# Optimization experiments

Measured on AMD Instinct MI355X. Metric: run time of the kernel, lower is better.

Reference implementation:

```python
import jax, jax.numpy as jnp
import numpy as np

T, B, H, L = 200, 32, 1024, 2
DROPOUT = 0.32
KEEP = 1.0 - DROPOUT
FORGET_GATE_BIAS = 1.0


def setup_inputs() -> dict:
    key = jax.random.key(0)
    ks = jax.random.split(key, 8)
    scale = 1.0 / np.sqrt(H)  # torch LSTM default init: U(-1/sqrt(H), 1/sqrt(H))
    x = jax.random.normal(ks[0], (T, B, H), jnp.float32)
    W_ih = jax.random.uniform(ks[1], (L, 4 * H, H), jnp.float32, -scale, scale)
    W_hh = jax.random.uniform(ks[2], (L, 4 * H, H), jnp.float32, -scale, scale)
    b_ih = jax.random.uniform(ks[3], (L, 4 * H), jnp.float32, -scale, scale)
    b_hh = jax.random.uniform(ks[4], (L, 4 * H), jnp.float32, -scale, scale)
    # forget-gate bias init as in LstmDrop.__init__ (gate order i,f,g,o)
    b_ih = b_ih.at[:, H:2 * H].set(FORGET_GATE_BIAS)
    b_hh = b_hh.at[:, H:2 * H].set(0.0)
    h0 = jnp.zeros((L, B, H), jnp.float32)
    c0 = jnp.zeros((L, B, H), jnp.float32)
    # inverted dropout masks: inter-layer (torch LSTM dropout, applied to all but last layer)
    # and the trailing inplace Dropout on the output sequence
    mask_inter = (jax.random.bernoulli(ks[5], KEEP, (L - 1, T, B, H)) / KEEP).astype(jnp.float32)
    mask_out = (jax.random.bernoulli(ks[6], KEEP, (T, B, H)) / KEEP).astype(jnp.float32)
    return {"x": x, "h0": h0, "c0": c0, "W_ih": W_ih, "W_hh": W_hh,
            "b_ih": b_ih, "b_hh": b_hh, "mask_inter": mask_inter, "mask_out": mask_out}


def _lstm_layer(xs, h, c, Wih, Whh, b):
    # xs: [T,B,in]; Wih/Whh: [4H,in]/[4H,H]; b: [4H] (b_ih + b_hh fused)
    def step(carry, x_t):
        h, c = carry
        gates = x_t @ Wih.T + h @ Whh.T + b  # [B,4H]
        i, f, g, o = jnp.split(gates, 4, axis=-1)
        c = jax.nn.sigmoid(f) * c + jax.nn.sigmoid(i) * jnp.tanh(g)
        h = jax.nn.sigmoid(o) * jnp.tanh(c)
        return (h, c), h
    (hT, cT), ys = jax.lax.scan(step, (h, c), xs)
    return ys, hT, cT


def reference(x, h0, c0, W_ih, W_hh, b_ih, b_hh, mask_inter, mask_out):
    y = x
    h_last, c_last = [], []
    for l in range(L):
        y, hT, cT = _lstm_layer(y, h0[l], c0[l], W_ih[l], W_hh[l], b_ih[l] + b_hh[l])
        h_last.append(hT)
        c_last.append(cT)
        if l < L - 1:  # torch LSTM applies dropout between layers only
            y = y * mask_inter[l]
    y = y * mask_out  # the inplace Dropout on the output sequence
    return y, jnp.stack(h_last), jnp.stack(c_last)
```

## Files before the change

kernel.cpp:

```cpp
#include <hip/hip_runtime.h>

#define T_STEPS 200
#define BATCH   32
#define HID     1024
#define NWG     256
#define NTHR    512

typedef _Float16 half8 __attribute__((ext_vector_type(8)));
typedef float    f32x4 __attribute__((ext_vector_type(4)));

__device__ __forceinline__ void st_coh16(_Float16* p, half8 v) {
    union { half8 h; unsigned long long u[2]; } r; r.h = v;
    unsigned long long* q = (unsigned long long*)p;
    __hip_atomic_store(q,     r.u[0], __ATOMIC_RELAXED, __HIP_MEMORY_SCOPE_AGENT);
    __hip_atomic_store(q + 1, r.u[1], __ATOMIC_RELAXED, __HIP_MEMORY_SCOPE_AGENT);
}

__device__ __forceinline__ half8 cvt8(const float* p) {
    f32x4 lo = *(const f32x4*)p;
    f32x4 hi = *(const f32x4*)(p + 4);
    half8 a;
    a[0] = (_Float16)lo[0]; a[1] = (_Float16)lo[1];
    a[2] = (_Float16)lo[2]; a[3] = (_Float16)lo[3];
    a[4] = (_Float16)hi[0]; a[5] = (_Float16)hi[1];
    a[6] = (_Float16)hi[2]; a[7] = (_Float16)hi[3];
    return a;
}

__global__ void init_k(const float* __restrict__ h0,
                       _Float16* __restrict__ h0b, _Float16* __restrict__ h1b,
                       unsigned* __restrict__ flag0, unsigned* __restrict__ flag1) {
    int i = blockIdx.x * blockDim.x + threadIdx.x;
    if (i < BATCH * HID) {
        h0b[i] = (_Float16)h0[i];
        h1b[i] = (_Float16)h0[BATCH * HID + i];
    }
    if (blockIdx.x == 0) {
        if (threadIdx.x < 128)      flag0[threadIdx.x * 32] = 0;
        else if (threadIdx.x < 256) flag1[(threadIdx.x - 128) * 32] = 0;
    }
}

__global__ __launch_bounds__(NTHR, 2) void lstm_main(
    const float* __restrict__ x, const float* __restrict__ c0,
    const float* __restrict__ Wih, const float* __restrict__ Whh,
    const float* __restrict__ bih, const float* __restrict__ bhh,
    const float* __restrict__ mi, const float* __restrict__ mo,
    float* __restrict__ out,
    _Float16* __restrict__ y0m, _Float16* __restrict__ h0b,
    _Float16* __restrict__ h1b, unsigned* __restrict__ flag0,
    unsigned* __restrict__ flag1)
{
    __shared__ _Float16 W_s[32 * 2048];
    __shared__ float scr[8][2][16][17];
    __shared__ float c_s[BATCH][8];
    __shared__ alignas(16) _Float16 st_h[BATCH][8];
    __shared__ alignas(16) _Float16 st_y[BATCH][8];
    __shared__ float st_o[BATCH][8];

    const int bid   = blockIdx.x;
    const int layer = bid >> 7;
    const int wgl   = bid & 127;
    const int tid   = threadIdx.x;

    const float* WihL = Wih + (size_t)layer * 4 * HID * HID;
    const float* WhhL = Whh + (size_t)layer * 4 * HID * HID;
    for (int idx = tid; idx < 32 * 2048; idx += NTHR) {
        int r = idx >> 11, k = idx & 2047;
        int grow = (r >> 3) * HID + wgl * 8 + (r & 7);
        float v = (k < HID) ? WihL[(size_t)grow * HID + k]
                            : WhhL[(size_t)grow * HID + (k - HID)];
        W_s[idx ^ ((r & 7) << 3)] = (_Float16)v;
    }

    float bias0 = 0.f, bias1 = 0.f, bias2 = 0.f, bias3 = 0.f;
    int b_ = 0, col_ = 0, gcol = 0;
    if (tid < 256) {
        b_ = tid >> 3; col_ = tid & 7; gcol = wgl * 8 + col_;
        bias0 = bih[layer * 4096 + gcol]           + bhh[layer * 4096 + gcol];
        bias1 = bih[layer * 4096 + HID + gcol]     + bhh[layer * 4096 + HID + gcol];
        bias2 = bih[layer * 4096 + 2 * HID + gcol] + bhh[layer * 4096 + 2 * HID + gcol];
        bias3 = bih[layer * 4096 + 3 * HID + gcol] + bhh[layer * 4096 + 3 * HID + gcol];
        c_s[b_][col_] = c0[((size_t)layer * BATCH + b_) * HID + gcol];
    }
    const int ot = tid - 256;
    const int b2 = (ot >= 0) ? (ot >> 3) : 0, c2 = (ot >= 0) ? (ot & 7) : 0;
    const int gcol2 = wgl * 8 + c2;
    __syncthreads();

    const int lane = tid & 63, wid = tid >> 6;
    int kq;
    if (layer == 0) kq = (wid < 4) ? (2 + (wid >> 1)) : ((wid - 4) >> 1);
    else            kq = wid >> 1;
    const int mm   = wid & 1;
    const int srow = kq * 2 + mm;
    const int row = lane & 15, bb = mm * 16 + row, ko = (lane >> 4) * 8;

    half8 aF[16];
    float mi_reg = 0.f, mo_reg = 0.f;
    if (layer == 0 && kq < 2) {
        const float* xp = x + (size_t)bb * HID + kq * 512 + ko;
        #pragma unroll
        for (int kk = 0; kk < 16; ++kk) aF[kk] = cvt8(xp + kk * 32);
    }
    if (layer == 1 && ot >= 0) mo_reg = mo[(size_t)b2 * HID + gcol2];

    for (int s = 0; s < T_STEPS; ++s) {
        if (layer == 0) {
            if (tid < 128) {
                const unsigned* f = flag0 + tid * 32;
                const unsigned tgt = (unsigned)s;
                while (__hip_atomic_load(f, __ATOMIC_RELAXED,
                                         __HIP_MEMORY_SCOPE_AGENT) < tgt) {}
            }
        } else {
            if (tid < 128) {
                const unsigned* f = flag0 + tid * 32;
                const unsigned tgt = (unsigned)(s + 1);
                while (__hip_atomic_load(f, __ATOMIC_RELAXED,
                                         __HIP_MEMORY_SCOPE_AGENT) < tgt) {}
            } else if (tid < 256) {
                const unsigned* f = flag1 + (tid - 128) * 32;
                const unsigned tgt = (unsigned)s;
                while (__hip_atomic_load(f, __ATOMIC_RELAXED,
                                         __HIP_MEMORY_SCOPE_AGENT) < tgt) {}
            }
        }
        asm volatile("" ::: "memory");
        __syncthreads();
        if (tid == 0) __builtin_amdgcn_fence(__ATOMIC_ACQUIRE, "agent");
        __syncthreads();

        if (layer == 0 && tid < 256)
            mi_reg = mi[((size_t)s * BATCH + b_) * HID + gcol];

        if (layer == 0) {
            if (kq >= 2) {
                const _Float16* hp = h0b + (s & 1) * (BATCH * HID)
                                   + bb * HID + (kq - 2) * 512 + ko;
                #pragma unroll
                for (int kk = 0; kk < 16; ++kk)
                    aF[kk] = *(const half8*)(hp + kk * 32);
            }
        } else {
            if (kq < 2) {
                const _Float16* yp = y0m + ((size_t)s * BATCH + bb) * HID + kq * 512 + ko;
                #pragma unroll
                for (int kk = 0; kk < 16; ++kk)
                    aF[kk] = *(const half8*)(yp + kk * 32);
            } else {
                const _Float16* hp = h1b + (s & 1) * (BATCH * HID)
                                   + bb * HID + (kq - 2) * 512 + ko;
                #pragma unroll
                for (int kk = 0; kk < 16; ++kk)
                    aF[kk] = *(const half8*)(hp + kk * 32);
            }
        }

        f32x4 acc0 = {0.f, 0.f, 0.f, 0.f}, acc1 = {0.f, 0.f, 0.f, 0.f};
        #pragma unroll
        for (int kk = 0; kk < 16; ++kk) {
            const int k  = kq * 512 + kk * 32 + ko;
            const int r1 = 16 + row;
            const half8 bB0 = *(const half8*)&W_s[(row * 2048 + k) ^ ((row & 7) << 3)];
            const half8 bB1 = *(const half8*)&W_s[(r1 * 2048 + k) ^ ((r1 & 7) << 3)];
            acc0 = __builtin_amdgcn_mfma_f32_16x16x32_f16(aF[kk], bB0, acc0, 0, 0, 0);
            acc1 = __builtin_amdgcn_mfma_f32_16x16x32_f16(aF[kk], bB1, acc1, 0, 0, 0);
        }
        #pragma unroll
        for (int j = 0; j < 4; ++j) {
            scr[srow][0][(lane >> 4) * 4 + j][row] = acc0[j];
            scr[srow][1][(lane >> 4) * 4 + j][row] = acc1[j];
        }
        __syncthreads();

        if (tid < 256) {
            const int m2 = b_ >> 4, rD = b_ & 15;
            float v0 = 0.f, v1 = 0.f, v2 = 0.f, v3 = 0.f;
            #pragma unroll
            for (int q = 0; q < 4; ++q) {
                v0 += scr[q * 2 + m2][0][rD][col_];
                v1 += scr[q * 2 + m2][0][rD][8 + col_];
                v2 += scr[q * 2 + m2][1][rD][col_];
                v3 += scr[q * 2 + m2][1][rD][8 + col_];
            }
            const float ig = 1.f / (1.f + __expf(-(v0 + bias0)));
            const float fg = 1.f / (1.f + __expf(-(v1 + bias1)));
            const float gg = tanhf(v2 + bias2);
            const float og = 1.f / (1.f + __expf(-(v3 + bias3)));
            const float cc = fg * c_s[b_][col_] + ig * gg;
            const float hh = og * tanhf(cc);
            c_s[b_][col_] = cc;

            st_h[b_][col_] = (_Float16)hh;
            if (layer == 0) st_y[b_][col_] = (_Float16)(hh * mi_reg);
            else            st_o[b_][col_] = hh;

            if (s == T_STEPS - 1) {
                const size_t base = (size_t)T_STEPS * BATCH * HID;
                __hip_atomic_store(&out[base + ((size_t)layer * BATCH + b_) * HID + gcol],
                                   hh, __ATOMIC_RELAXED, __HIP_MEMORY_SCOPE_AGENT);
                __hip_atomic_store(&out[base + (size_t)2 * BATCH * HID
                                        + ((size_t)layer * BATCH + b_) * HID + gcol],
                                   cc, __ATOMIC_RELAXED, __HIP_MEMORY_SCOPE_AGENT);
            }
        }
        __syncthreads();

        if (layer == 0) {
            if (wid >= 4) {
                if (tid >= 448 && tid < 480) {
                    const int sl = tid - 448;
                    st_coh16(&h0b[((s + 1) & 1) * (BATCH * HID) + sl * HID + wgl * 8],
                             *(const half8*)st_h[sl]);
                    st_coh16(&y0m[((size_t)s * BATCH + sl) * HID + wgl * 8],
                             *(const half8*)st_y[sl]);
                    asm volatile("s_waitcnt vmcnt(0)" ::: "memory");
                    if (tid == 448)
                        __hip_atomic_store(flag0 + wgl * 32, (unsigned)(s + 1),
                                           __ATOMIC_RELAXED, __HIP_MEMORY_SCOPE_AGENT);
                }
                if (kq < 2 && s + 1 < T_STEPS) {
                    const float* xp = x + ((size_t)(s + 1) * BATCH + bb) * HID + kq * 512 + ko;
                    #pragma unroll
                    for (int kk = 0; kk < 16; ++kk) aF[kk] = cvt8(xp + kk * 32);
                }
            }
        } else {
            if (ot >= 0) {
                __hip_atomic_store(&out[((size_t)s * BATCH + b2) * HID + gcol2],
                                   st_o[b2][c2] * mo_reg,
                                   __ATOMIC_RELAXED, __HIP_MEMORY_SCOPE_AGENT);
                if (tid >= 448 && tid < 480) {
                    const int sl = tid - 448;
                    st_coh16(&h1b[((s + 1) & 1) * (BATCH * HID) + sl * HID + wgl * 8],
                             *(const half8*)st_h[sl]);
                    asm volatile("s_waitcnt vmcnt(0)" ::: "memory");
                    if (tid == 448)
                        __hip_atomic_store(flag1 + wgl * 32, (unsigned)(s + 1),
                                           __ATOMIC_RELAXED, __HIP_MEMORY_SCOPE_AGENT);
                }
                if (s + 1 < T_STEPS)
                    mo_reg = mo[((size_t)(s + 1) * BATCH + b2) * HID + gcol2];
            }
        }
    }
}

extern "C" void kernel_launch(void* const* d_in, const int* in_sizes, int n_in,
                              void* d_out, int out_size, void* d_ws, size_t ws_size,
                              hipStream_t stream) {
    const float* x   = (const float*)d_in[0];
    const float* h0  = (const float*)d_in[1];
    const float* c0  = (const float*)d_in[2];
    const float* Wih = (const float*)d_in[3];
    const float* Whh = (const float*)d_in[4];
    const float* bih = (const float*)d_in[5];
    const float* bhh = (const float*)d_in[6];
    const float* mi  = (const float*)d_in[7];
    const float* mo  = (const float*)d_in[8];
    float* out = (float*)d_out;

    char* w = (char*)d_ws;
    _Float16* y0m   = (_Float16*)w;
    _Float16* h0b   = (_Float16*)(w + 13107200);
    _Float16* h1b   = (_Float16*)(w + 13107200 + 131072);
    unsigned* flag0 = (unsigned*)(w + 13107200 + 262144);
    unsigned* flag1 = (unsigned*)(w + 13107200 + 262144 + 16384);

    hipLaunchKernelGGL(init_k, dim3(128), dim3(256), 0, stream,
                       h0, h0b, h1b, flag0, flag1);

    void* args[] = {(void*)&x, (void*)&c0, (void*)&Wih, (void*)&Whh,
                    (void*)&bih, (void*)&bhh, (void*)&mi, (void*)&mo,
                    (void*)&out, (void*)&y0m, (void*)&h0b, (void*)&h1b,
                    (void*)&flag0, (void*)&flag1};
    hipLaunchCooperativeKernel((void*)lstm_main, dim3(NWG), dim3(NTHR),
                               args, 0, stream);
}
```

Baseline: 2.022 ms.

## Pack step flags contiguously and poll them with 64-bit wave-wide loads plus backoff

The per-workgroup progress flags were padded to one per 128-byte line and are now packed densely. Each polling thread reads two flags with a single 64-bit atomic load, so one wave covers all 128 flags. The wave leaves the loop only when every lane's flags have reached the target, and spins on a short ALU backoff between polls. The aim is fewer memory transactions and less L2 contention while spinning, at the cost of false sharing between writers on the same cache lines and extra wake-up latency from the backoff.

```diff
diff --git a/kernel.cpp b/kernel.cpp
--- a/kernel.cpp
+++ b/kernel.cpp
@@ -8,12 +8,16 @@
 
 typedef _Float16 half8 __attribute__((ext_vector_type(8)));
 typedef float    f32x4 __attribute__((ext_vector_type(4)));
+typedef unsigned long long u64;
+
+#define RLX __ATOMIC_RELAXED
+#define AGT __HIP_MEMORY_SCOPE_AGENT
 
 __device__ __forceinline__ void st_coh16(_Float16* p, half8 v) {
-    union { half8 h; unsigned long long u[2]; } r; r.h = v;
-    unsigned long long* q = (unsigned long long*)p;
-    __hip_atomic_store(q,     r.u[0], __ATOMIC_RELAXED, __HIP_MEMORY_SCOPE_AGENT);
-    __hip_atomic_store(q + 1, r.u[1], __ATOMIC_RELAXED, __HIP_MEMORY_SCOPE_AGENT);
+    union { half8 h; u64 u[2]; } r; r.h = v;
+    u64* q = (u64*)p;
+    __hip_atomic_store(q,     r.u[0], RLX, AGT);
+    __hip_atomic_store(q + 1, r.u[1], RLX, AGT);
 }
 
 __device__ __forceinline__ half8 cvt8(const float* p) {
@@ -27,6 +31,14 @@
     return a;
 }
 
+__device__ __forceinline__ void backoff() {
+    float jj = 1.0000001f;
+    #pragma unroll
+    for (int i = 0; i < 128; ++i)
+        asm volatile("v_fma_f32 %0,%0,%0,%0" : "+v"(jj));
+    asm volatile("" :: "v"(jj));
+}
+
 __global__ void init_k(const float* __restrict__ h0,
                        _Float16* __restrict__ h0b, _Float16* __restrict__ h1b,
                        unsigned* __restrict__ flag0, unsigned* __restrict__ flag1) {
@@ -35,9 +47,9 @@
         h0b[i] = (_Float16)h0[i];
         h1b[i] = (_Float16)h0[BATCH * HID + i];
     }
-    if (blockIdx.x == 0) {
-        if (threadIdx.x < 128)      flag0[threadIdx.x * 32] = 0;
-        else if (threadIdx.x < 256) flag1[(threadIdx.x - 128) * 32] = 0;
+    if (blockIdx.x == 0 && threadIdx.x < 128) {
+        flag0[threadIdx.x] = 0u;
+        flag1[threadIdx.x] = 0u;
     }
 }
 
@@ -107,23 +119,37 @@
 
     for (int s = 0; s < T_STEPS; ++s) {
         if (layer == 0) {
-            if (tid < 128) {
-                const unsigned* f = flag0 + tid * 32;
+            if (tid < 64) {
+                const u64* f = (const u64*)(flag0 + 2 * tid);
                 const unsigned tgt = (unsigned)s;
-                while (__hip_atomic_load(f, __ATOMIC_RELAXED,
-                                         __HIP_MEMORY_SCOPE_AGENT) < tgt) {}
+                const u64 tgt2 = ((u64)tgt << 32) | tgt;
+                for (;;) {
+                    u64 v = __hip_atomic_load(f, RLX, AGT);
+                    bool ok = ((unsigned)v >= tgt) && ((unsigned)(v >> 32) >= tgt);
+                    if (__all(ok)) break;
+                    backoff();
+                }
+                (void)tgt2;
             }
         } else {
-            if (tid < 128) {
-                const unsigned* f = flag0 + tid * 32;
+            if (tid < 64) {
+                const u64* f = (const u64*)(flag0 + 2 * tid);
                 const unsigned tgt = (unsigned)(s + 1);
-                while (__hip_atomic_load(f, __ATOMIC_RELAXED,
-                                         __HIP_MEMORY_SCOPE_AGENT) < tgt) {}
-            } else if (tid < 256) {
-                const unsigned* f = flag1 + (tid - 128) * 32;
+                for (;;) {
+                    u64 v = __hip_atomic_load(f, RLX, AGT);
+                    bool ok = ((unsigned)v >= tgt) && ((unsigned)(v >> 32) >= tgt);
+                    if (__all(ok)) break;
+                    backoff();
+                }
+            } else if (tid < 128) {
+                const u64* f = (const u64*)(flag1 + 2 * (tid - 64));
                 const unsigned tgt = (unsigned)s;
-                while (__hip_atomic_load(f, __ATOMIC_RELAXED,
-                                         __HIP_MEMORY_SCOPE_AGENT) < tgt) {}
+                for (;;) {
+                    u64 v = __hip_atomic_load(f, RLX, AGT);
+                    bool ok = ((unsigned)v >= tgt) && ((unsigned)(v >> 32) >= tgt);
+                    if (__all(ok)) break;
+                    backoff();
+                }
             }
         }
         asm volatile("" ::: "memory");
@@ -199,10 +225,10 @@
             if (s == T_STEPS - 1) {
                 const size_t base = (size_t)T_STEPS * BATCH * HID;
                 __hip_atomic_store(&out[base + ((size_t)layer * BATCH + b_) * HID + gcol],
-                                   hh, __ATOMIC_RELAXED, __HIP_MEMORY_SCOPE_AGENT);
+                                   hh, RLX, AGT);
                 __hip_atomic_store(&out[base + (size_t)2 * BATCH * HID
                                         + ((size_t)layer * BATCH + b_) * HID + gcol],
-                                   cc, __ATOMIC_RELAXED, __HIP_MEMORY_SCOPE_AGENT);
+                                   cc, RLX, AGT);
             }
         }
         __syncthreads();
@@ -217,8 +243,7 @@
                              *(const half8*)st_y[sl]);
                     asm volatile("s_waitcnt vmcnt(0)" ::: "memory");
                     if (tid == 448)
-                        __hip_atomic_store(flag0 + wgl * 32, (unsigned)(s + 1),
-                                           __ATOMIC_RELAXED, __HIP_MEMORY_SCOPE_AGENT);
+                        __hip_atomic_store(flag0 + wgl, (unsigned)(s + 1), RLX, AGT);
                 }
                 if (kq < 2 && s + 1 < T_STEPS) {
                     const float* xp = x + ((size_t)(s + 1) * BATCH + bb) * HID + kq * 512 + ko;
@@ -229,16 +254,14 @@
         } else {
             if (ot >= 0) {
                 __hip_atomic_store(&out[((size_t)s * BATCH + b2) * HID + gcol2],
-                                   st_o[b2][c2] * mo_reg,
-                                   __ATOMIC_RELAXED, __HIP_MEMORY_SCOPE_AGENT);
+                                   st_o[b2][c2] * mo_reg, RLX, AGT);
                 if (tid >= 448 && tid < 480) {
                     const int sl = tid - 448;
                     st_coh16(&h1b[((s + 1) & 1) * (BATCH * HID) + sl * HID + wgl * 8],
                              *(const half8*)st_h[sl]);
                     asm volatile("s_waitcnt vmcnt(0)" ::: "memory");
                     if (tid == 448)
-                        __hip_atomic_store(flag1 + wgl * 32, (unsigned)(s + 1),
-                                           __ATOMIC_RELAXED, __HIP_MEMORY_SCOPE_AGENT);
+                        __hip_atomic_store(flag1 + wgl, (unsigned)(s + 1), RLX, AGT);
                 }
                 if (s + 1 < T_STEPS)
                     mo_reg = mo[((size_t)(s + 1) * BATCH + b2) * HID + gcol2];
@@ -266,7 +289,7 @@
     _Float16* h0b   = (_Float16*)(w + 13107200);
     _Float16* h1b   = (_Float16*)(w + 13107200 + 131072);
     unsigned* flag0 = (unsigned*)(w + 13107200 + 262144);
-    unsigned* flag1 = (unsigned*)(w + 13107200 + 262144 + 16384);
+    unsigned* flag1 = (unsigned*)(w + 13107200 + 262144 + 1024);
 
     hipLaunchKernelGGL(init_k, dim3(128), dim3(256), 0, stream,
                        h0, h0b, h1b, flag0, flag1);
```

After: 2.739 ms. +35.4%, slower.

## Split each timestep into two batch halves with per-half flags for finer pipelining

Applied to the files above, without the earlier changes.

Each timestep now runs as two sub-steps over 16-row batch halves. Each half has its own flag set, so a consumer can start on one half while producers are still finishing the other, which lets layer 0 and layer 1 and the workgroups within each layer overlap more. Every wave now issues one MFMA chain per sub-step instead of two, and the gate math runs on 128 threads instead of 256. In exchange, each timestep does twice as many spin-waits and barriers.

```diff
diff --git a/kernel.cpp b/kernel.cpp
--- a/kernel.cpp
+++ b/kernel.cpp
@@ -3,27 +3,33 @@
 #define T_STEPS 200
 #define BATCH   32
 #define HID     1024
-#define NWG     256
 #define NTHR    512
+#define HB      (BATCH * HID)
 
 typedef _Float16 half8 __attribute__((ext_vector_type(8)));
 typedef float    f32x4 __attribute__((ext_vector_type(4)));
+typedef unsigned long long u64;
+
+#define RLX __ATOMIC_RELAXED
+#define AGT __HIP_MEMORY_SCOPE_AGENT
 
 __device__ __forceinline__ void st_coh16(_Float16* p, half8 v) {
-    union { half8 h; unsigned long long u[2]; } r; r.h = v;
-    unsigned long long* q = (unsigned long long*)p;
-    __hip_atomic_store(q,     r.u[0], __ATOMIC_RELAXED, __HIP_MEMORY_SCOPE_AGENT);
-    __hip_atomic_store(q + 1, r.u[1], __ATOMIC_RELAXED, __HIP_MEMORY_SCOPE_AGENT);
-}
+    union { half8 h; u64 u[2]; } r; r.h = v;
+    u64* q = (u64*)p;
+    __hip_atomic_store(q,     r.u[0], RLX, AGT);
+    __hip_atomic_store(q + 1, r.u[1], RLX, AGT);
+}
+static __device__ __forceinline__ unsigned lda32(const unsigned* p){
+    return __hip_atomic_load(p, RLX, AGT); }
+static __device__ __forceinline__ void sta32(unsigned* p, unsigned v){
+    __hip_atomic_store(p, v, RLX, AGT); }
 
 __device__ __forceinline__ half8 cvt8(const float* p) {
     f32x4 lo = *(const f32x4*)p;
     f32x4 hi = *(const f32x4*)(p + 4);
     half8 a;
-    a[0] = (_Float16)lo[0]; a[1] = (_Float16)lo[1];
-    a[2] = (_Float16)lo[2]; a[3] = (_Float16)lo[3];
-    a[4] = (_Float16)hi[0]; a[5] = (_Float16)hi[1];
-    a[6] = (_Float16)hi[2]; a[7] = (_Float16)hi[3];
+    a[0]=(_Float16)lo[0]; a[1]=(_Float16)lo[1]; a[2]=(_Float16)lo[2]; a[3]=(_Float16)lo[3];
+    a[4]=(_Float16)hi[0]; a[5]=(_Float16)hi[1]; a[6]=(_Float16)hi[2]; a[7]=(_Float16)hi[3];
     return a;
 }
 
@@ -31,14 +37,11 @@
                        _Float16* __restrict__ h0b, _Float16* __restrict__ h1b,
                        unsigned* __restrict__ flag0, unsigned* __restrict__ flag1) {
     int i = blockIdx.x * blockDim.x + threadIdx.x;
-    if (i < BATCH * HID) {
+    if (i < HB) {
         h0b[i] = (_Float16)h0[i];
-        h1b[i] = (_Float16)h0[BATCH * HID + i];
-    }
-    if (blockIdx.x == 0) {
-        if (threadIdx.x < 128)      flag0[threadIdx.x * 32] = 0;
-        else if (threadIdx.x < 256) flag1[(threadIdx.x - 128) * 32] = 0;
-    }
+        h1b[i] = (_Float16)h0[HB + i];
+    }
+    if (i < 8192) { flag0[i] = 0u; flag1[i] = 0u; }
 }
 
 __global__ __launch_bounds__(NTHR, 2) void lstm_main(
@@ -52,11 +55,11 @@
     unsigned* __restrict__ flag1)
 {
     __shared__ _Float16 W_s[32 * 2048];
-    __shared__ float scr[8][2][16][17];
+    __shared__ float scr[8][16][17];
     __shared__ float c_s[BATCH][8];
-    __shared__ alignas(16) _Float16 st_h[BATCH][8];
-    __shared__ alignas(16) _Float16 st_y[BATCH][8];
-    __shared__ float st_o[BATCH][8];
+    __shared__ alignas(16) _Float16 st_h[16][8];
+    __shared__ alignas(16) _Float16 st_y[16][8];
+    __shared__ float st_o[16][8];
 
     const int bid   = blockIdx.x;
     const int layer = bid >> 7;
@@ -73,175 +76,169 @@
         W_s[idx ^ ((r & 7) << 3)] = (_Float16)v;
     }
 
+    if (tid < 256) {
+        int b_ = tid >> 3, c_ = tid & 7;
+        c_s[b_][c_] = c0[((size_t)layer * BATCH + b_) * HID + wgl * 8 + c_];
+    }
+
     float bias0 = 0.f, bias1 = 0.f, bias2 = 0.f, bias3 = 0.f;
-    int b_ = 0, col_ = 0, gcol = 0;
-    if (tid < 256) {
-        b_ = tid >> 3; col_ = tid & 7; gcol = wgl * 8 + col_;
-        bias0 = bih[layer * 4096 + gcol]           + bhh[layer * 4096 + gcol];
-        bias1 = bih[layer * 4096 + HID + gcol]     + bhh[layer * 4096 + HID + gcol];
-        bias2 = bih[layer * 4096 + 2 * HID + gcol] + bhh[layer * 4096 + 2 * HID + gcol];
-        bias3 = bih[layer * 4096 + 3 * HID + gcol] + bhh[layer * 4096 + 3 * HID + gcol];
-        c_s[b_][col_] = c0[((size_t)layer * BATCH + b_) * HID + gcol];
-    }
-    const int ot = tid - 256;
-    const int b2 = (ot >= 0) ? (ot >> 3) : 0, c2 = (ot >= 0) ? (ot & 7) : 0;
-    const int gcol2 = wgl * 8 + c2;
+    int blA = 0, colA = 0, gcolA = 0;
+    if (tid < 128) {
+        blA = tid >> 3; colA = tid & 7; gcolA = wgl * 8 + colA;
+        bias0 = bih[layer*4096 + gcolA]          + bhh[layer*4096 + gcolA];
+        bias1 = bih[layer*4096 + HID + gcolA]    + bhh[layer*4096 + HID + gcolA];
+        bias2 = bih[layer*4096 + 2*HID + gcolA]  + bhh[layer*4096 + 2*HID + gcolA];
+        bias3 = bih[layer*4096 + 3*HID + gcolA]  + bhh[layer*4096 + 3*HID + gcolA];
+    }
+    const int ot  = tid - 256;
+    const int bO  = (ot >= 0 && ot < 128) ? (ot >> 3) : 0;
+    const int cO  = (ot >= 0 && ot < 128) ? (ot & 7) : 0;
     __syncthreads();
 
     const int lane = tid & 63, wid = tid >> 6;
     int kq;
     if (layer == 0) kq = (wid < 4) ? (2 + (wid >> 1)) : ((wid - 4) >> 1);
     else            kq = wid >> 1;
-    const int mm   = wid & 1;
-    const int srow = kq * 2 + mm;
-    const int row = lane & 15, bb = mm * 16 + row, ko = (lane >> 4) * 8;
+    const int half = wid & 1;
+    const int l15 = lane & 15, ko = (lane >> 4) * 8;
+    const int gr  = half * 16 + l15;
 
     half8 aF[16];
-    float mi_reg = 0.f, mo_reg = 0.f;
+    float mi_pf = 0.f, mo_pf = 0.f;
     if (layer == 0 && kq < 2) {
-        const float* xp = x + (size_t)bb * HID + kq * 512 + ko;
+        const float* xp = x + (size_t)l15 * HID + kq * 512 + ko;
         #pragma unroll
         for (int kk = 0; kk < 16; ++kk) aF[kk] = cvt8(xp + kk * 32);
     }
-    if (layer == 1 && ot >= 0) mo_reg = mo[(size_t)b2 * HID + gcol2];
+    if (layer == 0 && tid < 128) mi_pf = mi[(size_t)blA * HID + gcolA];
+    if (layer == 1 && ot >= 0 && ot < 128) mo_pf = mo[(size_t)bO * HID + wgl * 8 + cO];
 
     for (int s = 0; s < T_STEPS; ++s) {
-        if (layer == 0) {
+        for (int g = 0; g < 2; ++g) {
+            if (layer == 0) {
+                if (tid < 128) {
+                    const unsigned* f = flag0 + (size_t)(g * 128 + tid) * 32;
+                    while (lda32(f) < (unsigned)s) {}
+                }
+            } else {
+                if (tid < 128) {
+                    const unsigned* f = flag0 + (size_t)(g * 128 + tid) * 32;
+                    while (lda32(f) < (unsigned)(s + 1)) {}
+                } else if (tid < 256) {
+                    const unsigned* f = flag1 + (size_t)(g * 128 + tid - 128) * 32;
+                    while (lda32(f) < (unsigned)s) {}
+                }
+            }
+            asm volatile("" ::: "memory");
+            __syncthreads();
+            if (tid == 0) __builtin_amdgcn_fence(__ATOMIC_ACQUIRE, "agent");
+            __syncthreads();
+
+            if (layer == 0) {
+                if (kq >= 2) {
+                    const _Float16* hp = h0b + (size_t)(s & 1) * HB
+                                       + (size_t)(g * 16 + l15) * HID + (kq - 2) * 512 + ko;
+                    #pragma unroll
+                    for (int kk = 0; kk < 16; ++kk) aF[kk] = *(const half8*)(hp + kk * 32);
+                }
+            } else {
+                if (kq < 2) {
+                    const _Float16* yp = y0m + ((size_t)s * BATCH + g * 16 + l15) * HID
+                                       + kq * 512 + ko;
+                    #pragma unroll
+                    for (int kk = 0; kk < 16; ++kk) aF[kk] = *(const half8*)(yp + kk * 32);
+                } else {
+                    const _Float16* hp = h1b + (size_t)(s & 1) * HB
+                                       + (size_t)(g * 16 + l15) * HID + (kq - 2) * 512 + ko;
+                    #pragma unroll
+                    for (int kk = 0; kk < 16; ++kk) aF[kk] = *(const half8*)(hp + kk * 32);
+                }
+            }
+
+            f32x4 acc = {0.f, 0.f, 0.f, 0.f};
+            #pragma unroll
+            for (int kk = 0; kk < 16; ++kk) {
+                const int k = kq * 512 + kk * 32 + ko;
+                const half8 bB = *(const half8*)&W_s[(gr * 2048 + k) ^ ((gr & 7) << 3)];
+                acc = __builtin_amdgcn_mfma_f32_16x16x32_f16(aF[kk], bB, acc, 0, 0, 0);
+            }
+            #pragma unroll
+            for (int j = 0; j < 4; ++j)
+                scr[wid][(lane >> 4) * 4 + j][l15] = acc[j];
+            __syncthreads();
+
             if (tid < 128) {
-                const unsigned* f = flag0 + tid * 32;
-                const unsigned tgt = (unsigned)s;
-                while (__hip_atomic_load(f, __ATOMIC_RELAXED,
-                                         __HIP_MEMORY_SCOPE_AGENT) < tgt) {}
-            }
-        } else {
-            if (tid < 128) {
-                const unsigned* f = flag0 + tid * 32;
-                const unsigned tgt = (unsigned)(s + 1);
-                while (__hip_atomic_load(f, __ATOMIC_RELAXED,
-                                         __HIP_MEMORY_SCOPE_AGENT) < tgt) {}
-            } else if (tid < 256) {
-                const unsigned* f = flag1 + (tid - 128) * 32;
-                const unsigned tgt = (unsigned)s;
-                while (__hip_atomic_load(f, __ATOMIC_RELAXED,
-                                         __HIP_MEMORY_SCOPE_AGENT) < tgt) {}
-            }
-        }
-        asm volatile("" ::: "memory");
-        __syncthreads();
-        if (tid == 0) __builtin_amdgcn_fence(__ATOMIC_ACQUIRE, "agent");
-        __syncthreads();
-
-        if (layer == 0 && tid < 256)
-            mi_reg = mi[((size_t)s * BATCH + b_) * HID + gcol];
-
-        if (layer == 0) {
-            if (kq >= 2) {
-                const _Float16* hp = h0b + (s & 1) * (BATCH * HID)
-                                   + bb * HID + (kq - 2) * 512 + ko;
-                #pragma unroll
-                for (int kk = 0; kk < 16; ++kk)
-                    aF[kk] = *(const half8*)(hp + kk * 32);
-            }
-        } else {
-            if (kq < 2) {
-                const _Float16* yp = y0m + ((size_t)s * BATCH + bb) * HID + kq * 512 + ko;
-                #pragma unroll
-                for (int kk = 0; kk < 16; ++kk)
-                    aF[kk] = *(const half8*)(yp + kk * 32);
+                float v0 = scr[0][blA][colA]   + scr[2][blA][colA]
+                         + scr[4][blA][colA]   + scr[6][blA][colA];
+                float v1 = scr[0][blA][8+colA] + scr[2][blA][8+colA]
+                         + scr[4][blA][8+colA] + scr[6][blA][8+colA];
+                float v2 = scr[1][blA][colA]   + scr[3][blA][colA]
+                         + scr[5][blA][colA]   + scr[7][blA][colA];
+                float v3 = scr[1][blA][8+colA] + scr[3][blA][8+colA]
+                         + scr[5][blA][8+colA] + scr[7][blA][8+colA];
+                const float ig = 1.f / (1.f + __expf(-(v0 + bias0)));
+                const float fg = 1.f / (1.f + __expf(-(v1 + bias1)));
+                const float gg = tanhf(v2 + bias2);
+                const float og = 1.f / (1.f + __expf(-(v3 + bias3)));
+                const int gb = g * 16 + blA;
+                const float cc = fg * c_s[gb][colA] + ig * gg;
+                const float hh = og * tanhf(cc);
+                c_s[gb][colA] = cc;
+
+                st_h[blA][colA] = (_Float16)hh;
+                if (layer == 0) st_y[blA][colA] = (_Float16)(hh * mi_pf);
+                else            st_o[blA][colA] = hh;
+
+                if (s == T_STEPS - 1) {
+                    const size_t base = (size_t)T_STEPS * BATCH * HID;
+                    out[base + ((size_t)layer * BATCH + gb) * HID + gcolA] = hh;
+                    out[base + (size_t)2 * BATCH * HID
+                        + ((size_t)layer * BATCH + gb) * HID + gcolA] = cc;
+                }
+            }
+            __syncthreads();
+
+            const int gn = g ^ 1;
+            const int sn = s + (g == 1);
+            if (layer == 0) {
+                if (wid == 7) {
+                    if (lane < 16) {
+                        st_coh16(&h0b[(size_t)((s + 1) & 1) * HB
+                                      + (size_t)(g * 16 + lane) * HID + wgl * 8],
+                                 *(const half8*)st_h[lane]);
+                    } else if (lane < 32) {
+                        st_coh16(&y0m[((size_t)s * BATCH + g * 16 + lane - 16) * HID + wgl * 8],
+                                 *(const half8*)st_y[lane - 16]);
+                    }
+                    asm volatile("s_waitcnt vmcnt(0)" ::: "memory");
+                    if (lane == 0)
+                        sta32(flag0 + (size_t)(g * 128 + wgl) * 32, (unsigned)(s + 1));
+                }
+                if (wid >= 4 && kq < 2 && sn < T_STEPS) {
+                    const float* xp = x + ((size_t)sn * BATCH + gn * 16 + l15) * HID
+                                    + kq * 512 + ko;
+                    #pragma unroll
+                    for (int kk = 0; kk < 16; ++kk) aF[kk] = cvt8(xp + kk * 32);
+                }
+                if (tid < 128 && sn < T_STEPS)
+                    mi_pf = mi[((size_t)sn * BATCH + gn * 16 + blA) * HID + gcolA];
             } else {
-                const _Float16* hp = h1b + (s & 1) * (BATCH * HID)
-                                   + bb * HID + (kq - 2) * 512 + ko;
-                #pragma unroll
-                for (int kk = 0; kk < 16; ++kk)
-                    aF[kk] = *(const half8*)(hp + kk * 32);
-            }
-        }
-
-        f32x4 acc0 = {0.f, 0.f, 0.f, 0.f}, acc1 = {0.f, 0.f, 0.f, 0.f};
-        #pragma unroll
-        for (int kk = 0; kk < 16; ++kk) {
-            const int k  = kq * 512 + kk * 32 + ko;
-            const int r1 = 16 + row;
-            const half8 bB0 = *(const half8*)&W_s[(row * 2048 + k) ^ ((row & 7) << 3)];
-            const half8 bB1 = *(const half8*)&W_s[(r1 * 2048 + k) ^ ((r1 & 7) << 3)];
-            acc0 = __builtin_amdgcn_mfma_f32_16x16x32_f16(aF[kk], bB0, acc0, 0, 0, 0);
-            acc1 = __builtin_amdgcn_mfma_f32_16x16x32_f16(aF[kk], bB1, acc1, 0, 0, 0);
-        }
-        #pragma unroll
-        for (int j = 0; j < 4; ++j) {
-            scr[srow][0][(lane >> 4) * 4 + j][row] = acc0[j];
-            scr[srow][1][(lane >> 4) * 4 + j][row] = acc1[j];
-        }
-        __syncthreads();
-
-        if (tid < 256) {
-            const int m2 = b_ >> 4, rD = b_ & 15;
-            float v0 = 0.f, v1 = 0.f, v2 = 0.f, v3 = 0.f;
-            #pragma unroll
-            for (int q = 0; q < 4; ++q) {
-                v0 += scr[q * 2 + m2][0][rD][col_];
-                v1 += scr[q * 2 + m2][0][rD][8 + col_];
-                v2 += scr[q * 2 + m2][1][rD][col_];
-                v3 += scr[q * 2 + m2][1][rD][8 + col_];
-            }
-            const float ig = 1.f / (1.f + __expf(-(v0 + bias0)));
-            const float fg = 1.f / (1.f + __expf(-(v1 + bias1)));
-            const float gg = tanhf(v2 + bias2);
-            const float og = 1.f / (1.f + __expf(-(v3 + bias3)));
-            const float cc = fg * c_s[b_][col_] + ig * gg;
-            const float hh = og * tanhf(cc);
-            c_s[b_][col_] = cc;
-
-            st_h[b_][col_] = (_Float16)hh;
-            if (layer == 0) st_y[b_][col_] = (_Float16)(hh * mi_reg);
-            else            st_o[b_][col_] = hh;
-
-            if (s == T_STEPS - 1) {
-                const size_t base = (size_t)T_STEPS * BATCH * HID;
-                __hip_atomic_store(&out[base + ((size_t)layer * BATCH + b_) * HID + gcol],
-                                   hh, __ATOMIC_RELAXED, __HIP_MEMORY_SCOPE_AGENT);
-                __hip_atomic_store(&out[base + (size_t)2 * BATCH * HID
-                                        + ((size_t)layer * BATCH + b_) * HID + gcol],
-                                   cc, __ATOMIC_RELAXED, __HIP_MEMORY_SCOPE_AGENT);
-            }
-        }
-        __syncthreads();
-
-        if (layer == 0) {
-            if (wid >= 4) {
-                if (tid >= 448 && tid < 480) {
-                    const int sl = tid - 448;
-                    st_coh16(&h0b[((s + 1) & 1) * (BATCH * HID) + sl * HID + wgl * 8],
-                             *(const half8*)st_h[sl]);
-                    st_coh16(&y0m[((size_t)s * BATCH + sl) * HID + wgl * 8],
-                             *(const half8*)st_y[sl]);
+                if (wid == 7) {
+                    if (lane < 16) {
+                        st_coh16(&h1b[(size_t)((s + 1) & 1) * HB
+                                      + (size_t)(g * 16 + lane) * HID + wgl * 8],
+                                 *(const half8*)st_h[lane]);
+                    }
                     asm volatile("s_waitcnt vmcnt(0)" ::: "memory");
-                    if (tid == 448)
-                        __hip_atomic_store(flag0 + wgl * 32, (unsigned)(s + 1),
-                                           __ATOMIC_RELAXED, __HIP_MEMORY_SCOPE_AGENT);
-                }
-                if (kq < 2 && s + 1 < T_STEPS) {
-                    const float* xp = x + ((size_t)(s + 1) * BATCH + bb) * HID + kq * 512 + ko;
-                    #pragma unroll
-                    for (int kk = 0; kk < 16; ++kk) aF[kk] = cvt8(xp + kk * 32);
-                }
-            }
-        } else {
-            if (ot >= 0) {
-                __hip_atomic_store(&out[((size_t)s * BATCH + b2) * HID + gcol2],
-                                   st_o[b2][c2] * mo_reg,
-                                   __ATOMIC_RELAXED, __HIP_MEMORY_SCOPE_AGENT);
-                if (tid >= 448 && tid < 480) {
-                    const int sl = tid - 448;
-                    st_coh16(&h1b[((s + 1) & 1) * (BATCH * HID) + sl * HID + wgl * 8],
-                             *(const half8*)st_h[sl]);
-                    asm volatile("s_waitcnt vmcnt(0)" ::: "memory");
-                    if (tid == 448)
-                        __hip_atomic_store(flag1 + wgl * 32, (unsigned)(s + 1),
-                                           __ATOMIC_RELAXED, __HIP_MEMORY_SCOPE_AGENT);
-                }
-                if (s + 1 < T_STEPS)
-                    mo_reg = mo[((size_t)(s + 1) * BATCH + b2) * HID + gcol2];
+                    if (lane == 0)
+                        sta32(flag1 + (size_t)(g * 128 + wgl) * 32, (unsigned)(s + 1));
+                }
+                if (ot >= 0 && ot < 128) {
+                    out[((size_t)s * BATCH + g * 16 + bO) * HID + wgl * 8 + cO]
+                        = st_o[bO][cO] * mo_pf;
+                    if (sn < T_STEPS)
+                        mo_pf = mo[((size_t)sn * BATCH + gn * 16 + bO) * HID + wgl * 8 + cO];
+                }
             }
         }
     }
@@ -264,9 +261,9 @@
     char* w = (char*)d_ws;
     _Float16* y0m   = (_Float16*)w;
     _Float16* h0b   = (_Float16*)(w + 13107200);
-    _Float16* h1b   = (_Float16*)(w + 13107200 + 131072);
-    unsigned* flag0 = (unsigned*)(w + 13107200 + 262144);
-    unsigned* flag1 = (unsigned*)(w + 13107200 + 262144 + 16384);
+    _Float16* h1b   = (_Float16*)(w + 13238272);
+    unsigned* flag0 = (unsigned*)(w + 13369344);
+    unsigned* flag1 = (unsigned*)(w + 13402112);
 
     hipLaunchKernelGGL(init_k, dim3(128), dim3(256), 0, stream,
                        h0, h0b, h1b, flag0, flag1);
@@ -275,6 +272,6 @@
                     (void*)&bih, (void*)&bhh, (void*)&mi, (void*)&mo,
                     (void*)&out, (void*)&y0m, (void*)&h0b, (void*)&h1b,
                     (void*)&flag0, (void*)&flag1};
-    hipLaunchCooperativeKernel((void*)lstm_main, dim3(NWG), dim3(NTHR),
+    hipLaunchCooperativeKernel((void*)lstm_main, dim3(256), dim3(NTHR),
                                args, 0, stream);
 }
```

Result: slower. 3.344 ms (+65.4%).
